# Kernel optimization log

Measured on AMD Instinct MI355X. Metric: run time of the kernel, lower is better.

Reference implementation:

```python
import jax, jax.numpy as jnp
import numpy as np

I, T, L, E, H, W = 256, 256, 32, 128, 7, 7
INIT_TEMPERATURE = 0.07


def setup_inputs() -> dict:
    key = jax.random.key(0)
    k1, k2, k3 = jax.random.split(key, 3)
    image_features = jax.random.normal(k1, (I, E, H, W), dtype=jnp.float32)
    text_features = jax.random.normal(k2, (T, L, E), dtype=jnp.float32)
    # valid caption lengths in [1, L] (avoid zero to prevent div-by-zero)
    text_length = jax.random.randint(k3, (T,), 1, L + 1, dtype=jnp.int32)
    logit_neg_log_temperature = jnp.asarray(-np.log(INIT_TEMPERATURE), dtype=jnp.float32)
    return {
        "image_features": image_features,
        "text_features": text_features,
        "text_length": text_length,
        "logit_neg_log_temperature": logit_neg_log_temperature,
    }


def reference(image_features, text_features, text_length, logit_neg_log_temperature):
    # image_features: [I, E, H, W]; text_features: [T, L, E]
    # per-(image, text, word) similarity over spatial positions: [I, T, L, H, W]
    match_max = jnp.einsum("iehw,tle->itlhw", image_features, text_features)
    # max over spatial dims (h, w): [I, T, L]
    match_max = jnp.max(match_max, axis=(3, 4))
    # sum over words, normalize by caption length: [I, T]
    match = jnp.sum(match_max, axis=2) / text_length.astype(match_max.dtype)
    logit_scale = jnp.exp(logit_neg_log_temperature)
    logits_per_image = match * logit_scale
    logits_per_text = match.T * logit_scale
    return (logits_per_image, logits_per_text)
```

## Files before the change

### kernel.cpp

```cpp
#include <hip/hip_runtime.h>

typedef int   v8i    __attribute__((ext_vector_type(8)));
typedef float f32x16 __attribute__((ext_vector_type(16)));

#define NI 256
#define NT 256
#define NL 32
#define NE 128
#define HW 49
#define NEG_INF (-3.0e38f)
#define SCALE1 0x7F7F7F7F


__device__ __forceinline__ unsigned char f32_to_e4m3(float f)
{
    unsigned fb = __float_as_uint(f);
    unsigned s  = (fb >> 24) & 0x80;
    int      e  = (int)((fb >> 23) & 0xFF);
    unsigned m  = fb & 0x7FFFFF;
    int ne = e - 120;
    if (ne <= 0)  return (unsigned char)s;
    if (ne > 15) { ne = 15; m = 0x600000; }
    unsigned base = ((unsigned)ne << 3) | (m >> 20);
    unsigned rem  = m & 0xFFFFF;
    if (rem > 0x80000 || (rem == 0x80000 && (base & 1))) base++;
    if (base > 0x7E) base = 0x7E;
    return (unsigned char)(s | base);
}

__global__ __launch_bounds__(256, 4)
void prep_kernel(const float* __restrict__ img,
                 const float* __restrict__ txt,
                 unsigned char* __restrict__ wsA,
                 unsigned char* __restrict__ wsB)
{
    const int tid  = threadIdx.x;
    const int wave = tid >> 6, lane = tid & 63;
    const int ml   = lane & 31, h = lane >> 5;
    const int bid  = blockIdx.x;
    if (bid < 1024) {
        int gw = bid;
        int i  = gw >> 2, mt = (gw >> 1) & 1, ks = gw & 1;
        int m  = mt * 32 + ml; if (m > HW - 1) m = HW - 1;
        int e0 = ks * 64 + h * 32 + wave * 8;
        const float* p = img + ((size_t)i * NE + e0) * HW + m;
        union { unsigned char b[8]; int2 v; } u;
        #pragma unroll
        for (int j = 0; j < 8; ++j) u.b[j] = f32_to_e4m3(p[j * HW]);
        *(int2*)(wsA + (size_t)gw * 2048 + lane * 32 + wave * 8) = u.v;
    } else {
        int bb = bid - 1024;
        int gw = bb * 2 + (wave >> 1);
        int eh = wave & 1;
        int t  = gw >> 1, ks = gw & 1;
        int e0 = ks * 64 + h * 32 + eh * 16;
        const float* p = txt + ((size_t)t * NL + ml) * NE + e0;
        union { unsigned char b[16]; int4 v; } u;
        #pragma unroll
        for (int q = 0; q < 4; ++q) {
            float4 f = *(const float4*)(p + q * 4);
            u.b[q*4+0] = f32_to_e4m3(f.x); u.b[q*4+1] = f32_to_e4m3(f.y);
            u.b[q*4+2] = f32_to_e4m3(f.z); u.b[q*4+3] = f32_to_e4m3(f.w);
        }
        *(int4*)(wsB + (size_t)gw * 2048 + eh * 1024 + lane * 16) = u.v;
    }
}

#define GLDS(gp, lp) __builtin_amdgcn_global_load_lds(                     \
        (const __attribute__((address_space(1))) void*)(gp),               \
        (__attribute__((address_space(3))) void*)(lp), 16, 0, 0)

__global__ __launch_bounds__(256, 4)
void clip_match_kernel(const unsigned char* __restrict__ wsA,
                       const unsigned char* __restrict__ wsB,
                       const int* __restrict__ tlen,
                       const float* __restrict__ nlt,
                       float* __restrict__ out)
{
    const int tid  = threadIdx.x;
    const int wave = tid >> 6, lane = tid & 63;
    const int ml   = lane & 31, h = lane >> 5;
    const int tb   = blockIdx.x & 15;
    const int ig   = blockIdx.x >> 4;
    const int im   = ig * 4 + wave;

    __shared__ __align__(16) unsigned char bstage[32768];
    __shared__ __align__(16) float colmax[4][16][32];

    const unsigned char* pa = wsA + (size_t)im * 8192 + lane * 32;
    v8i aA0 = *(const v8i*)(pa);
    v8i aA1 = *(const v8i*)(pa + 2048);
    v8i aB0 = *(const v8i*)(pa + 4096);
    v8i aB1 = *(const v8i*)(pa + 6144);

    const unsigned char* csrc = wsB + (size_t)tb * 16 * 4096;

#define COMPUTE(bk0, bk1, t)                                                \
    {                                                                       \
        f32x16 acc0 = __builtin_amdgcn_mfma_scale_f32_32x32x64_f8f6f4(      \
            aA0, bk0, (f32x16)(0.f), 0, 0, 0, SCALE1, 0, SCALE1);           \
        acc0 = __builtin_amdgcn_mfma_scale_f32_32x32x64_f8f6f4(             \
            aA1, bk1, acc0, 0, 0, 0, SCALE1, 0, SCALE1);                    \
        f32x16 acc1 = __builtin_amdgcn_mfma_scale_f32_32x32x64_f8f6f4(      \
            aB0, bk0, (f32x16)(0.f), 0, 0, 0, SCALE1, 0, SCALE1);           \
        acc1 = __builtin_amdgcn_mfma_scale_f32_32x32x64_f8f6f4(             \
            aB1, bk1, acc1, 0, 0, 0, SCALE1, 0, SCALE1);                    \
           \
        float t0[8];                                                        \
        _Pragma("unroll")                                                   \
        for (int k = 0; k < 8; ++k) t0[k] = fmaxf(acc0[2*k], acc0[2*k+1]);  \
        float t1[4];                                                        \
        _Pragma("unroll")                                                   \
        for (int k = 0; k < 4; ++k) t1[k] = fmaxf(t0[2*k], t0[2*k+1]);      \
        float a0m = fmaxf(fmaxf(t1[0], t1[1]), fmaxf(t1[2], t1[3]));        \
        float u0[4];                                                        \
        _Pragma("unroll")                                                   \
        for (int k = 0; k < 4; ++k) u0[k] = fmaxf(acc1[2*k], acc1[2*k+1]);  \
        float a1m = fmaxf(fmaxf(u0[0], u0[1]), fmaxf(u0[2], u0[3]));        \
        float ex  = (h == 0) ? acc1[8] : NEG_INF;                           \
        float cm  = fmaxf(fmaxf(a0m, a1m), ex);                             \
        cm = fmaxf(cm, __shfl_xor(cm, 32));             \
        if (h == 0) colmax[wave][t][ml] = cm;                               \
    }

    #pragma unroll 1
    for (int r = 0; r < 2; ++r) {
        {
            const unsigned char* src = csrc + r * 32768;
            #pragma unroll
            for (int it = 0; it < 8; ++it)
                GLDS(src + it * 4096 + tid * 16, bstage + it * 4096 + tid * 16);
        }
        asm volatile("s_waitcnt vmcnt(0)" ::: "memory");
        __builtin_amdgcn_sched_barrier(0);
        __syncthreads();

        #pragma unroll
        for (int ts = 0; ts < 8; ++ts) {
            const int t = r * 8 + ts;
            union { int4 q[2]; v8i v; } b0, b1;
            const unsigned char* base = bstage + ts * 4096 + lane * 16;
            b0.q[0] = *(const int4*)(base);
            b0.q[1] = *(const int4*)(base + 1024);
            b1.q[0] = *(const int4*)(base + 2048);
            b1.q[1] = *(const int4*)(base + 3072);
            COMPUTE(b0.v, b1.v, t)
        }
        __syncthreads();
    }

    {
        const float scale = expf(nlt[0]);
        const int t = lane & 15;
        const int q = lane >> 4;
        const float* row = &colmax[wave][t][q * 8];
        float4 a0 = *(const float4*)(row + 0);
        float4 a1 = *(const float4*)(row + 4);
        float s = ((a0.x + a0.y) + (a0.z + a0.w))
                + ((a1.x + a1.y) + (a1.z + a1.w));
        s += __shfl_xor(s, 16);
        s += __shfl_xor(s, 32);
        if (q == 0) {
            int tg = tb * 16 + t;
            float v = s * scale / (float)tlen[tg];
            out[im * NT + tg] = v;
            out[NI * NT + tg * NI + im] = v;
        }
    }
}

extern "C" void kernel_launch(void* const* d_in, const int* in_sizes, int n_in,
                              void* d_out, int out_size, void* d_ws, size_t ws_size,
                              hipStream_t stream)
{
    const float* img  = (const float*)d_in[0];
    const float* txt  = (const float*)d_in[1];
    const int*   tlen = (const int*)d_in[2];
    const float* nlt  = (const float*)d_in[3];
    float* out = (float*)d_out;

    unsigned char* wsA = (unsigned char*)d_ws;
    unsigned char* wsB = wsA + (size_t)2 * 1024 * 1024;

    prep_kernel<<<dim3(1280), dim3(256), 0, stream>>>(img, txt, wsA, wsB);
    clip_match_kernel<<<dim3(1024), dim3(256), 0, stream>>>(wsA, wsB, tlen, nlt, out);
}
```

Baseline: 27.40 us.

## Fuse FP8 conversion into the match kernel and drop the prep kernel

Removes the separate prep kernel and its workspace round trip. Each block now loads its 4 images' fp32 features into LDS, converts them to e4m3 in the MFMA fragment layout, and converts its text tile from fp32 to fp8 inline. This saves one kernel launch and the global write and read of the converted operands. In exchange it repeats the conversion redundantly, since each image is converted by 16 blocks and each text by 64, and it adds LDS staging and barriers.

```diff
diff --git a/kernel.cpp b/kernel.cpp
--- a/kernel.cpp
+++ b/kernel.cpp
@@ -29,50 +29,8 @@
 }
 
 __global__ __launch_bounds__(256, 4)
-void prep_kernel(const float* __restrict__ img,
-                 const float* __restrict__ txt,
-                 unsigned char* __restrict__ wsA,
-                 unsigned char* __restrict__ wsB)
-{
-    const int tid  = threadIdx.x;
-    const int wave = tid >> 6, lane = tid & 63;
-    const int ml   = lane & 31, h = lane >> 5;
-    const int bid  = blockIdx.x;
-    if (bid < 1024) {
-        int gw = bid;
-        int i  = gw >> 2, mt = (gw >> 1) & 1, ks = gw & 1;
-        int m  = mt * 32 + ml; if (m > HW - 1) m = HW - 1;
-        int e0 = ks * 64 + h * 32 + wave * 8;
-        const float* p = img + ((size_t)i * NE + e0) * HW + m;
-        union { unsigned char b[8]; int2 v; } u;
-        #pragma unroll
-        for (int j = 0; j < 8; ++j) u.b[j] = f32_to_e4m3(p[j * HW]);
-        *(int2*)(wsA + (size_t)gw * 2048 + lane * 32 + wave * 8) = u.v;
-    } else {
-        int bb = bid - 1024;
-        int gw = bb * 2 + (wave >> 1);
-        int eh = wave & 1;
-        int t  = gw >> 1, ks = gw & 1;
-        int e0 = ks * 64 + h * 32 + eh * 16;
-        const float* p = txt + ((size_t)t * NL + ml) * NE + e0;
-        union { unsigned char b[16]; int4 v; } u;
-        #pragma unroll
-        for (int q = 0; q < 4; ++q) {
-            float4 f = *(const float4*)(p + q * 4);
-            u.b[q*4+0] = f32_to_e4m3(f.x); u.b[q*4+1] = f32_to_e4m3(f.y);
-            u.b[q*4+2] = f32_to_e4m3(f.z); u.b[q*4+3] = f32_to_e4m3(f.w);
-        }
-        *(int4*)(wsB + (size_t)gw * 2048 + eh * 1024 + lane * 16) = u.v;
-    }
-}
-
-#define GLDS(gp, lp) __builtin_amdgcn_global_load_lds(                     \
-        (const __attribute__((address_space(1))) void*)(gp),               \
-        (__attribute__((address_space(3))) void*)(lp), 16, 0, 0)
-
-__global__ __launch_bounds__(256, 4)
-void clip_match_kernel(const unsigned char* __restrict__ wsA,
-                       const unsigned char* __restrict__ wsB,
+void clip_fused_kernel(const float* __restrict__ img,
+                       const float* __restrict__ txt,
                        const int* __restrict__ tlen,
                        const float* __restrict__ nlt,
                        float* __restrict__ out)
@@ -80,20 +38,51 @@
     const int tid  = threadIdx.x;
     const int wave = tid >> 6, lane = tid & 63;
     const int ml   = lane & 31, h = lane >> 5;
-    const int tb   = blockIdx.x & 15;
-    const int ig   = blockIdx.x >> 4;
+    const int bid  = blockIdx.x;
+    const int tb   = bid >> 6;
+    const int ig   = bid & 63;
     const int im   = ig * 4 + wave;
 
-    __shared__ __align__(16) unsigned char bstage[32768];
-    __shared__ __align__(16) float colmax[4][16][32];
+    __shared__ __align__(16) unsigned char lds_all[40960];
+    float*         scratch = (float*)lds_all;
+    unsigned char* Aout    = lds_all + 25600;
+    unsigned char* bstage  = lds_all;
+    float (*colmax)[16][32] = (float(*)[16][32])(lds_all + 32768);
 
-    const unsigned char* pa = wsA + (size_t)im * 8192 + lane * 32;
-    v8i aA0 = *(const v8i*)(pa);
-    v8i aA1 = *(const v8i*)(pa + 2048);
-    v8i aB0 = *(const v8i*)(pa + 4096);
-    v8i aB1 = *(const v8i*)(pa + 6144);
-
-    const unsigned char* csrc = wsB + (size_t)tb * 16 * 4096;
+    v8i aA0, aA1, aB0, aB1;
+    #pragma unroll
+    for (int r4 = 0; r4 < 4; ++r4) {
+        const int p     = (r4 + (tb & 3)) & 3;
+        const int image = ig * 4 + p;
+        const float4* src4 = (const float4*)(img + (size_t)image * (NE * HW));
+        #pragma unroll
+        for (int q = 0; q < 7; ++q) {
+            int idx = tid + 256 * q;
+            if (idx < 1568) ((float4*)scratch)[idx] = src4[idx];
+        }
+        __syncthreads();
+        {
+            int fi = tid >> 6, l = tid & 63;
+            int mt = fi >> 1, ksg = fi & 1;
+            int m  = mt * 32 + (l & 31); if (m > HW - 1) m = HW - 1;
+            int e0 = ksg * 64 + (l >> 5) * 32;
+            union { unsigned char b[32]; int4 v[2]; } ug;
+            #pragma unroll
+            for (int j = 0; j < 32; ++j)
+                ug.b[j] = f32_to_e4m3(scratch[(e0 + j) * HW + m]);
+            *(int4*)(Aout + fi * 2048 + l * 32)      = ug.v[0];
+            *(int4*)(Aout + fi * 2048 + l * 32 + 16) = ug.v[1];
+        }
+        __syncthreads();
+        if (wave == p) {
+            const unsigned char* pa = Aout + lane * 32;
+            aA0 = *(const v8i*)(pa);
+            aA1 = *(const v8i*)(pa + 2048);
+            aB0 = *(const v8i*)(pa + 4096);
+            aB1 = *(const v8i*)(pa + 6144);
+        }
+    }
+    __syncthreads();
 
 #define COMPUTE(bk0, bk1, t)                                                \
     {                                                                       \
@@ -125,14 +114,27 @@
 
     #pragma unroll 1
     for (int r = 0; r < 2; ++r) {
-        {
-            const unsigned char* src = csrc + r * 32768;
+        #pragma unroll
+        for (int q = 0; q < 4; ++q) {
+            int s     = tid + 256 * q;
+            int t_loc = (((s >> 7) + ig) & 7);
+            int rest  = s & 127;
+            int ksb   = rest >> 6;
+            int l     = rest & 63;
+            int t     = tb * 16 + r * 8 + t_loc;
+            const float* pb = txt + ((size_t)t * NL + (l & 31)) * NE
+                                  + ksb * 64 + (l >> 5) * 32;
+            union { unsigned char b[32]; int4 v[2]; } ub;
             #pragma unroll
-            for (int it = 0; it < 8; ++it)
-                GLDS(src + it * 4096 + tid * 16, bstage + it * 4096 + tid * 16);
+            for (int w = 0; w < 8; ++w) {
+                float4 f = *(const float4*)(pb + w * 4);
+                ub.b[w*4+0] = f32_to_e4m3(f.x); ub.b[w*4+1] = f32_to_e4m3(f.y);
+                ub.b[w*4+2] = f32_to_e4m3(f.z); ub.b[w*4+3] = f32_to_e4m3(f.w);
+            }
+            unsigned char* dst = bstage + t_loc * 4096 + ksb * 2048;
+            *(int4*)(dst + l * 16)        = ub.v[0];
+            *(int4*)(dst + 1024 + l * 16) = ub.v[1];
         }
-        asm volatile("s_waitcnt vmcnt(0)" ::: "memory");
-        __builtin_amdgcn_sched_barrier(0);
         __syncthreads();
 
         #pragma unroll
@@ -148,6 +150,7 @@
         }
         __syncthreads();
     }
+#undef COMPUTE
 
     {
         const float scale = expf(nlt[0]);
@@ -179,9 +182,6 @@
     const float* nlt  = (const float*)d_in[3];
     float* out = (float*)d_out;
 
-    unsigned char* wsA = (unsigned char*)d_ws;
-    unsigned char* wsB = wsA + (size_t)2 * 1024 * 1024;
-
-    prep_kernel<<<dim3(1280), dim3(256), 0, stream>>>(img, txt, wsA, wsB);
-    clip_match_kernel<<<dim3(1024), dim3(256), 0, stream>>>(wsA, wsB, tlen, nlt, out);
+    clip_fused_kernel<<<dim3(1024), dim3(256), 0, stream>>>(
+        img, txt, tlen, nlt, out);
 }
```

New measurement: 90.39 us. 3.3x slower.

## Stage image tiles through LDS with coalesced nontemporal loads in prep kernel

Applied to the files above, without the earlier changes.

The prep kernel now gives each block one image. The block loads that image's 128x49 float slab into shared memory with coalesced, nontemporal 16-byte loads, then transposes and converts it to FP8 from LDS. Previously each thread did strided global reads. Text conversion now uses one block per caption with nontemporal loads, and the grid drops from 1280 to 512 blocks. The cost is a 25 KB LDS footprint per block, lower occupancy (launch bounds 2), and likely LDS bank conflicts on the strided transpose reads.

```diff
diff --git a/kernel.cpp b/kernel.cpp
--- a/kernel.cpp
+++ b/kernel.cpp
@@ -2,6 +2,7 @@
 
 typedef int   v8i    __attribute__((ext_vector_type(8)));
 typedef float f32x16 __attribute__((ext_vector_type(16)));
+typedef float f32x4v __attribute__((ext_vector_type(4)));
 
 #define NI 256
 #define NT 256
@@ -28,41 +29,53 @@
     return (unsigned char)(s | base);
 }
 
-__global__ __launch_bounds__(256, 4)
+__global__ __launch_bounds__(256, 2)
 void prep_kernel(const float* __restrict__ img,
                  const float* __restrict__ txt,
                  unsigned char* __restrict__ wsA,
                  unsigned char* __restrict__ wsB)
 {
-    const int tid  = threadIdx.x;
-    const int wave = tid >> 6, lane = tid & 63;
-    const int ml   = lane & 31, h = lane >> 5;
-    const int bid  = blockIdx.x;
-    if (bid < 1024) {
-        int gw = bid;
-        int i  = gw >> 2, mt = (gw >> 1) & 1, ks = gw & 1;
-        int m  = mt * 32 + ml; if (m > HW - 1) m = HW - 1;
-        int e0 = ks * 64 + h * 32 + wave * 8;
-        const float* p = img + ((size_t)i * NE + e0) * HW + m;
-        union { unsigned char b[8]; int2 v; } u;
-        #pragma unroll
-        for (int j = 0; j < 8; ++j) u.b[j] = f32_to_e4m3(p[j * HW]);
-        *(int2*)(wsA + (size_t)gw * 2048 + lane * 32 + wave * 8) = u.v;
+    const int tid = threadIdx.x;
+    const int bid = blockIdx.x;
+
+    if (bid < 256) {
+        __shared__ __align__(16) float scratch[NE * HW];
+        const int i = bid;
+        const f32x4v* src4 = (const f32x4v*)(img + (size_t)i * (NE * HW));
+        #pragma unroll
+        for (int q = 0; q < 7; ++q) {
+            int idx = tid + 256 * q;
+            if (idx < (NE * HW) / 4)
+                ((f32x4v*)scratch)[idx] = __builtin_nontemporal_load(src4 + idx);
+        }
+        __syncthreads();
+        const int fi = tid >> 6, l = tid & 63;
+        const int mt = fi >> 1, ks = fi & 1;
+        int m  = mt * 32 + (l & 31); if (m > HW - 1) m = HW - 1;
+        const int e0 = ks * 64 + (l >> 5) * 32;
+        union { unsigned char b[32]; int4 v[2]; } u;
+        #pragma unroll
+        for (int j = 0; j < 32; ++j)
+            u.b[j] = f32_to_e4m3(scratch[(e0 + j) * HW + m]);
+        unsigned char* dst = wsA + (size_t)(i * 4 + fi) * 2048 + l * 32;
+        *(int4*)(dst)      = u.v[0];
+        *(int4*)(dst + 16) = u.v[1];
     } else {
-        int bb = bid - 1024;
-        int gw = bb * 2 + (wave >> 1);
-        int eh = wave & 1;
-        int t  = gw >> 1, ks = gw & 1;
-        int e0 = ks * 64 + h * 32 + eh * 16;
-        const float* p = txt + ((size_t)t * NL + ml) * NE + e0;
+        const int t   = bid - 256;
+        const int ks  = tid >> 7;
+        const int rem = tid & 127;
+        const int eh  = rem >> 6;
+        const int l   = rem & 63;
+        const int e0  = ks * 64 + (l >> 5) * 32 + eh * 16;
+        const float* p = txt + ((size_t)t * NL + (l & 31)) * NE + e0;
         union { unsigned char b[16]; int4 v; } u;
         #pragma unroll
         for (int q = 0; q < 4; ++q) {
-            float4 f = *(const float4*)(p + q * 4);
+            f32x4v f = __builtin_nontemporal_load((const f32x4v*)(p + q * 4));
             u.b[q*4+0] = f32_to_e4m3(f.x); u.b[q*4+1] = f32_to_e4m3(f.y);
             u.b[q*4+2] = f32_to_e4m3(f.z); u.b[q*4+3] = f32_to_e4m3(f.w);
         }
-        *(int4*)(wsB + (size_t)gw * 2048 + eh * 1024 + lane * 16) = u.v;
+        *(int4*)(wsB + (size_t)(t * 2 + ks) * 2048 + eh * 1024 + l * 16) = u.v;
     }
 }
 
@@ -182,6 +195,6 @@
     unsigned char* wsA = (unsigned char*)d_ws;
     unsigned char* wsB = wsA + (size_t)2 * 1024 * 1024;
 
-    prep_kernel<<<dim3(1280), dim3(256), 0, stream>>>(img, txt, wsA, wsB);
+    prep_kernel<<<dim3(512), dim3(256), 0, stream>>>(img, txt, wsA, wsB);
     clip_match_kernel<<<dim3(1024), dim3(256), 0, stream>>>(wsA, wsB, tlen, nlt, out);
 }
```

After: 29.01 us. +5.9%, slower.
